# Kernel tuning notes

Hardware: AMD Instinct MI355X
Metric: run time of the kernel (lower is better)

The kernel has to match this reference:

```python
import jax, jax.numpy as jnp
import numpy as np


def setup_inputs() -> dict:
    key = jax.random.key(0)
    k1, k2, k3, k4 = jax.random.split(key, 4)
    B, S, D_IN, D_OUT = 4, 4096, 768, 128
    x = jax.random.normal(k1, (B, S, D_IN), dtype=jnp.float32)
    # torch Linear(d_in, d_out) weight is [d_out, d_in]; we store transposed [d_in, d_out]
    scale = 1.0 / np.sqrt(D_IN)
    Wq = jax.random.normal(k2, (D_IN, D_OUT), dtype=jnp.float32) * scale
    Wk = jax.random.normal(k3, (D_IN, D_OUT), dtype=jnp.float32) * scale
    Wv = jax.random.normal(k4, (D_IN, D_OUT), dtype=jnp.float32) * scale
    return {"x": x, "Wq": Wq, "Wk": Wk, "Wv": Wv}


def reference(x, Wq, Wk, Wv):
    # x: [B, S, d_in]; Wq/Wk/Wv: [d_in, d_out]
    B, S, _ = x.shape
    q = jnp.einsum('bsd,de->bse', x, Wq)
    k = jnp.einsum('bsd,de->bse', x, Wk)
    v = jnp.einsum('bsd,de->bse', x, Wv)
    d_out = k.shape[-1]
    scores = jnp.einsum('bqe,bke->bqk', q, k)  # [B, S, S]
    causal = jnp.tril(jnp.ones((S, S), dtype=bool))  # True where attention allowed
    scores = jnp.where(causal[None], scores, -jnp.inf)
    attn = jax.nn.softmax(scores / jnp.sqrt(jnp.float32(d_out)), axis=-1)
    # dropout prob is 0.0 -> identity
    return jnp.einsum('bqk,bke->bqe', attn, v)
```

## Files before the change

kernel.cpp:

```cpp
#include <hip/hip_runtime.h>
#include <stdint.h>

typedef unsigned short u16;
typedef uint32_t u32;
typedef __bf16 bf16;
typedef bf16 bf16x8 __attribute__((ext_vector_type(8)));
typedef float f32x4 __attribute__((ext_vector_type(4)));
typedef uint32_t u32x4 __attribute__((ext_vector_type(4)));

#define S_LEN 4096
#define D_IN 768
#define D_OUT 128
#define NB 4
#define M_TOTAL (NB * S_LEN)

static __device__ __forceinline__ u16 f2bf(float f) {
    union { float f; uint32_t u; } c; c.f = f;
    return (u16)((c.u + 0x7FFFu + ((c.u >> 16) & 1u)) >> 16);
}
static __device__ __forceinline__ float bf2f_lo(uint32_t w) { return __uint_as_float(w << 16); }
static __device__ __forceinline__ float bf2f_hi(uint32_t w) { return __uint_as_float(w & 0xFFFF0000u); }

static __device__ __forceinline__ bf16x8 ld8(const u16* p) {
    union { u32x4 v; bf16x8 b; } c;
    c.v = *reinterpret_cast<const u32x4*>(p);
    return c.b;
}

static __device__ __forceinline__ f32x4 mfma16(bf16x8 a, bf16x8 b, f32x4 c) {
    return __builtin_amdgcn_mfma_f32_16x16x32_bf16(a, b, c, 0, 0, 0);
}

static __device__ __forceinline__ void gload16(const void* g, void* l) {
    __builtin_amdgcn_global_load_lds((const __attribute__((address_space(1))) uint32_t*)g,
                                     (__attribute__((address_space(3))) uint32_t*)l, 16, 0, 0);
}

static __device__ __forceinline__ float bpermf(int addr, float v) {
    return __int_as_float(__builtin_amdgcn_ds_bpermute(addr, __float_as_int(v)));
}
static __device__ __forceinline__ u32 bpermu(int addr, u32 v) {
    return (u32)__builtin_amdgcn_ds_bpermute(addr, (int)v);
}
static __device__ __forceinline__ u32 pk2(float a, float b) {
    return __builtin_amdgcn_perm(__float_as_uint(b), __float_as_uint(a), 0x07060302u);
}

__global__ __launch_bounds__(256) void wt_kernel(const float* __restrict__ Wq, const float* __restrict__ Wk,
                                                 const float* __restrict__ Wv, u16* __restrict__ Wt) {
    __shared__ u16 tl[128][40];
    const int w = blockIdx.x / 24;
    const int kc = (blockIdx.x % 24) * 32;
    const float* W = (w == 0) ? Wq : (w == 1) ? Wk : Wv;
#pragma unroll
    for (int p = 0; p < 4; ++p) {
        int kr = p * 8 + (threadIdx.x >> 5);
        int nc = (threadIdx.x & 31) * 4;
        float4 v = *reinterpret_cast<const float4*>(W + (size_t)(kc + kr) * D_OUT + nc);
        tl[nc + 0][kr] = f2bf(v.x); tl[nc + 1][kr] = f2bf(v.y);
        tl[nc + 2][kr] = f2bf(v.z); tl[nc + 3][kr] = f2bf(v.w);
    }
    __syncthreads();
    const int n = threadIdx.x >> 1, kh = (threadIdx.x & 1) * 16;
    u32x4* dst = reinterpret_cast<u32x4*>(Wt + (size_t)w * D_OUT * D_IN + (size_t)n * D_IN + kc + kh);
    const u32x4* src = reinterpret_cast<const u32x4*>(&tl[n][kh]);
    dst[0] = src[0];
    dst[1] = src[1];
}

__global__ __launch_bounds__(256) void qkv_kernel(const float* __restrict__ x, const u16* __restrict__ Wt,
                                                  u16* __restrict__ Qb, u16* __restrict__ Kb,
                                                  u16* __restrict__ Vt) {
    __shared__ __align__(16) u16 wslab[2][192 * 32];
    __shared__ __align__(16) float xslab[2][64 * 32];
    const int wave = threadIdx.x >> 6, lane = threadIdx.x & 63;
    const int r = lane & 15, g = lane >> 4;
    const int m0 = blockIdx.x * 64;
    const int h = blockIdx.y;

    f32x4 acc[3][4];
#pragma unroll
    for (int y = 0; y < 3; ++y)
#pragma unroll
        for (int f = 0; f < 4; ++f) acc[y][f] = f32x4{0.f, 0.f, 0.f, 0.f};

    auto stageW = [&](int bb, int kk) {
#pragma unroll
        for (int i = 0; i < 3; ++i) {
            int c = i * 4 + wave;
            int rr = c * 16 + (lane >> 2);
            int gr = (rr >> 6) * 128 + h * 64 + (rr & 63);
            const u16* src = Wt + (size_t)gr * D_IN + kk * 32 + (((lane & 3) ^ (rr & 3)) * 8);
            gload16(src, &wslab[bb][c * 512]);
        }
    };
    auto stageX = [&](int bb, int kk) {
#pragma unroll
        for (int i = 0; i < 2; ++i) {
            int c = i * 4 + wave;
            int row = c * 8 + (lane >> 3);
            const float* src = x + (size_t)(m0 + row) * D_IN + kk * 32 + (((lane & 7) ^ (row & 7)) * 4);
            gload16(src, &xslab[bb][c * 256]);
        }
    };

    stageW(0, 0);
    stageX(0, 0);
    int buf = 0;
    const int arow = wave * 16 + r;
    for (int kk = 0; kk < 24; ++kk) {
        int kn = (kk + 1 < 24) ? kk + 1 : 0;
        stageX(buf ^ 1, kn);
        stageW(buf ^ 1, kn);
        asm volatile("s_waitcnt vmcnt(5)" ::: "memory");
        __builtin_amdgcn_sched_barrier(0);
        __builtin_amdgcn_s_barrier();
        f32x4 xa0 = *reinterpret_cast<const f32x4*>(&xslab[buf][arow * 32 + (((2 * g) ^ (arow & 7)) * 4)]);
        f32x4 xa1 = *reinterpret_cast<const f32x4*>(&xslab[buf][arow * 32 + (((2 * g + 1) ^ (arow & 7)) * 4)]);
        union { u16 u[8]; bf16x8 bv; } af;
#pragma unroll
        for (int t = 0; t < 4; ++t) { af.u[t] = f2bf(xa0[t]); af.u[4 + t] = f2bf(xa1[t]); }
#pragma unroll
        for (int y = 0; y < 3; ++y)
#pragma unroll
            for (int f = 0; f < 4; ++f) {
                int rr = y * 64 + f * 16 + r;
                bf16x8 wf = ld8(&wslab[buf][rr * 32 + ((g ^ (r & 3)) * 8)]);
                acc[y][f] = mfma16(af.bv, wf, acc[y][f]);
            }
        __builtin_amdgcn_s_barrier();
        buf ^= 1;
    }
    asm volatile("s_waitcnt vmcnt(0)" ::: "memory");

    const float QSC = 0.1275174366f;
#pragma unroll
    for (int f = 0; f < 4; ++f)
#pragma unroll
        for (int i = 0; i < 4; ++i) {
            int mrow = m0 + wave * 16 + 4 * g + i;
            int col = h * 64 + f * 16 + r;
            Qb[(size_t)mrow * D_OUT + col] = f2bf(acc[0][f][i] * QSC);
            Kb[(size_t)mrow * D_OUT + col] = f2bf(acc[1][f][i]);
            Vt[((size_t)((mrow >> 12) * D_OUT + col)) * S_LEN + (mrow & 4095)] = f2bf(acc[2][f][i]);
        }
}

__global__ __launch_bounds__(512, 2) void attn_kernel(const u16* __restrict__ Qb, const u16* __restrict__ Kb,
                                                      const u16* __restrict__ Vt, u16* __restrict__ Po,
                                                      float* __restrict__ Pml, float* __restrict__ out,
                                                      int nsplit) {
    __shared__ __align__(16) u16 kbuf[2][64 * 128];
    __shared__ __align__(16) u16 vbuf[2][128 * 64];

    const int wave = threadIdx.x >> 6, lane = threadIdx.x & 63;
    const int r = lane & 15, g = lane >> 4;
    const int n = (int)blockIdx.x;
    const int b = (n & 7) >> 1;
    const int rem = ((n >> 3) << 1) | (n & 1);
    const int s = rem >> 4;
    const int xh = rem & 15;
    const int t = (2 * s < nsplit) ? (15 - xh) : xh;
    const int nj = 4 * t + 4;
    if (s >= nj) return;
    const int qw0 = t * 256 + wave * 32;

    const u16* Kp = Kb + (size_t)b * S_LEN * D_OUT;
    const u16* Vp = Vt + (size_t)b * D_OUT * S_LEN;

    bf16x8 qf[2][4];
#pragma unroll
    for (int rb = 0; rb < 2; ++rb)
#pragma unroll
        for (int kk = 0; kk < 4; ++kk)
            qf[rb][kk] = ld8(Qb + ((size_t)(b * S_LEN + qw0 + rb * 16 + r)) * D_OUT + kk * 32 + 8 * g);

    f32x4 o[2][8];
    float l_[2];
#pragma unroll
    for (int rb = 0; rb < 2; ++rb) {
#pragma unroll
        for (int f = 0; f < 8; ++f) o[rb][f] = f32x4{0.f, 0.f, 0.f, 0.f};
        l_[rb] = 0.f;
    }

    const int la4 = (r + 32 * (g & 1)) * 4;
    const int lb4 = la4 + 64;
    const int lx16 = (lane ^ 16) * 4, lx32 = (lane ^ 32) * 4;
    const bool hi = (g >= 2);

    auto stageK = [&](int bb, int k0) {
#pragma unroll
        for (int i = 0; i < 2; ++i) {
            int c = i * 8 + wave;
            int row = c * 4 + (lane >> 4);
            const u16* src = Kp + (size_t)(k0 + row) * D_OUT + (((lane & 15) ^ (row & 7)) * 8);
            gload16(src, &kbuf[bb][c * 512]);
        }
    };
    auto stageV = [&](int bb, int k0) {
#pragma unroll
        for (int i = 0; i < 2; ++i) {
            int c = i * 8 + wave;
            int row = c * 8 + (lane >> 3);
            const u16* src = Vp + (size_t)row * S_LEN + k0 + (((lane & 7) ^ (row & 7)) * 8);
            gload16(src, &vbuf[bb][c * 512]);
        }
    };

    stageK(0, s * 64);
    stageV(0, s * 64);
    int buf = 0;
    for (int j = s; j < nj; j += nsplit) {
        const int k0 = j * 64;
        const int j2 = j + nsplit;
        const int kn = (j2 < nj) ? j2 * 64 : s * 64;
        stageK(buf ^ 1, kn);
        stageV(buf ^ 1, kn);
        asm volatile("s_waitcnt vmcnt(4)" ::: "memory");
        __builtin_amdgcn_sched_barrier(0);
        __builtin_amdgcn_s_barrier();

        f32x4 sv[2][4];
#pragma unroll
        for (int rb = 0; rb < 2; ++rb)
#pragma unroll
            for (int f = 0; f < 4; ++f) sv[rb][f] = f32x4{0.f, 0.f, 0.f, 0.f};
        __builtin_amdgcn_s_setprio(1);
#pragma unroll
        for (int kk = 0; kk < 4; ++kk)
#pragma unroll
            for (int f = 0; f < 4; ++f) {
                bf16x8 kf = ld8(&kbuf[buf][(f * 16 + r) * 128 + (((kk * 4 + g) ^ (r & 7)) * 8)]);
                sv[0][f] = mfma16(kf, qf[0][kk], sv[0][f]);
                sv[1][f] = mfma16(kf, qf[1][kk], sv[1][f]);
            }
        __builtin_amdgcn_s_setprio(0);

        bf16x8 pb[2][2];
#pragma unroll
        for (int rb = 0; rb < 2; ++rb) {
            const int qrb = qw0 + rb * 16;
            const int q = qrb + r;
            if (k0 + 63 > qrb) {
#pragma unroll
                for (int f = 0; f < 4; ++f)
#pragma unroll
                    for (int i = 0; i < 4; ++i)
                        if (k0 + 16 * f + 4 * g + i > q) sv[rb][f][i] = -1e30f;
            }
            float r0 = 0.f;
#pragma unroll
            for (int f = 0; f < 4; ++f)
#pragma unroll
                for (int i = 0; i < 4; ++i) {
                    float p = __builtin_amdgcn_exp2f(sv[rb][f][i]);
                    sv[rb][f][i] = p;
                    r0 += p;
                }
            l_[rb] += r0;

            u32 pkl[4], pkh[4];
#pragma unroll
            for (int f = 0; f < 4; ++f) {
                pkl[f] = pk2(sv[rb][f][0], sv[rb][f][1]);
                pkh[f] = pk2(sv[rb][f][2], sv[rb][f][3]);
            }
#pragma unroll
            for (int kk2 = 0; kk2 < 2; ++kk2) {
                const int f1 = 2 * kk2, f2 = 2 * kk2 + 1;
                u32 a1 = bpermu(la4, pkl[f1]), a2 = bpermu(la4, pkl[f2]);
                u32 b1 = bpermu(la4, pkh[f1]), b2 = bpermu(la4, pkh[f2]);
                u32 c1 = bpermu(lb4, pkl[f1]), c2 = bpermu(lb4, pkl[f2]);
                u32 d1 = bpermu(lb4, pkh[f1]), d2 = bpermu(lb4, pkh[f2]);
                union { u32x4 u; bf16x8 bv; } cc;
                cc.u = u32x4{hi ? a2 : a1, hi ? b2 : b1, hi ? c2 : c1, hi ? d2 : d1};
                pb[rb][kk2] = cc.bv;
            }
        }

        __builtin_amdgcn_s_setprio(1);
#pragma unroll
        for (int kk2 = 0; kk2 < 2; ++kk2)
#pragma unroll
            for (int f = 0; f < 8; ++f) {
                bf16x8 vf = ld8(&vbuf[buf][(f * 16 + r) * 64 + (((kk2 * 4 + g) ^ (r & 7)) * 8)]);
                o[0][f] = mfma16(vf, pb[0][kk2], o[0][f]);
                o[1][f] = mfma16(vf, pb[1][kk2], o[1][f]);
            }
        __builtin_amdgcn_s_setprio(0);
        __builtin_amdgcn_s_barrier();
        buf ^= 1;
    }
    asm volatile("s_waitcnt vmcnt(0)" ::: "memory");

    l_[0] += bpermf(lx16, l_[0]);
    l_[1] += bpermf(lx16, l_[1]);
    l_[0] += bpermf(lx32, l_[0]);
    l_[1] += bpermf(lx32, l_[1]);

    if (nsplit == 1) {
#pragma unroll
        for (int rb = 0; rb < 2; ++rb) {
            float inv = 1.0f / l_[rb];
            float* orow = out + ((size_t)(b * S_LEN + qw0 + rb * 16 + r)) * D_OUT;
#pragma unroll
            for (int f = 0; f < 8; ++f) {
                float4 v;
                v.x = o[rb][f][0] * inv; v.y = o[rb][f][1] * inv;
                v.z = o[rb][f][2] * inv; v.w = o[rb][f][3] * inv;
                *reinterpret_cast<float4*>(orow + 16 * f + 4 * g) = v;
            }
        }
    } else {
        const int pt = (b * 16 + t) * nsplit + s;
        u16* po = Po + (size_t)pt * (256 * 128);
        float* pml = Pml + (size_t)pt * 512;
#pragma unroll
        for (int rb = 0; rb < 2; ++rb) {
            u16* chunk0 = po + (size_t)((wave * 2 + rb) * 8) * 256 + lane * 4;
#pragma unroll
            for (int f = 0; f < 8; ++f) {
                u32 w0 = (u32)f2bf(o[rb][f][0]) | ((u32)f2bf(o[rb][f][1]) << 16);
                u32 w1 = (u32)f2bf(o[rb][f][2]) | ((u32)f2bf(o[rb][f][3]) << 16);
                uint2 ww; ww.x = w0; ww.y = w1;
                *reinterpret_cast<uint2*>(chunk0 + f * 256) = ww;
            }
            if (g == 0) {
                const int row = wave * 32 + rb * 16 + r;
                pml[row * 2 + 0] = 0.f;
                pml[row * 2 + 1] = l_[rb];
            }
        }
    }
}

__global__ __launch_bounds__(256) void merge_kernel(const u16* __restrict__ Po, const float* __restrict__ Pml,
                                                    float* __restrict__ out, int nsplit) {
    const int gr = blockIdx.x * 16 + (threadIdx.x >> 4);
    const int c0 = (threadIdx.x & 15) * 8;
    const int b = gr >> 12, rr = gr & 4095;
    const int t = rr >> 8, row = rr & 255;
    const int ns = min(nsplit, 4 * t + 4);
    const size_t pbase = (size_t)(b * 16 + t) * nsplit;

    const int wv = row >> 5, rbm = (row >> 4) & 1, r_ = row & 15;
    const int fm = c0 >> 4, g0 = (c0 >> 2) & 3;
    const size_t coff = (size_t)((wv * 2 + rbm) * 8 + fm) * 256;

    float L = 0.f;
#pragma unroll
    for (int s = 0; s < 8; ++s)
        if (s < ns) L += Pml[(pbase + s) * 512 + row * 2 + 1];
    const float inv = 1.0f / L;

    float acc[8];
#pragma unroll
    for (int k = 0; k < 8; ++k) acc[k] = 0.f;
#pragma unroll
    for (int s = 0; s < 8; ++s) {
        if (s < ns) {
            const u16* chunk = Po + (pbase + s) * (256 * 128) + coff;
            uint2 pv0 = *reinterpret_cast<const uint2*>(chunk + (g0 * 16 + r_) * 4);
            uint2 pv1 = *reinterpret_cast<const uint2*>(chunk + ((g0 + 1) * 16 + r_) * 4);
            acc[0] += bf2f_lo(pv0.x); acc[1] += bf2f_hi(pv0.x);
            acc[2] += bf2f_lo(pv0.y); acc[3] += bf2f_hi(pv0.y);
            acc[4] += bf2f_lo(pv1.x); acc[5] += bf2f_hi(pv1.x);
            acc[6] += bf2f_lo(pv1.y); acc[7] += bf2f_hi(pv1.y);
        }
    }
    float* op = out + (size_t)gr * D_OUT + c0;
    float4 v0, v1;
    v0.x = acc[0] * inv; v0.y = acc[1] * inv; v0.z = acc[2] * inv; v0.w = acc[3] * inv;
    v1.x = acc[4] * inv; v1.y = acc[5] * inv; v1.z = acc[6] * inv; v1.w = acc[7] * inv;
    *reinterpret_cast<float4*>(op) = v0;
    *reinterpret_cast<float4*>(op + 4) = v1;
}

extern "C" void kernel_launch(void* const* d_in, const int* in_sizes, int n_in,
                              void* d_out, int out_size, void* d_ws, size_t ws_size,
                              hipStream_t stream) {
    const float* x  = (const float*)d_in[0];
    const float* Wq = (const float*)d_in[1];
    const float* Wk = (const float*)d_in[2];
    const float* Wv = (const float*)d_in[3];
    float* out = (float*)d_out;

    u16* Qb = (u16*)d_ws;
    u16* Kb = Qb + (size_t)M_TOTAL * D_OUT;
    u16* Vt = Kb + (size_t)M_TOTAL * D_OUT;
    u16* Wt = Vt + (size_t)M_TOTAL * D_OUT;

    const unsigned long long base = (3ULL * M_TOTAL * D_OUT + 3ULL * D_OUT * D_IN) * 2ULL;
    const unsigned long long per = 4325376ULL;
    int nsplit = 8;
    if (ws_size < base + 8ULL * per) nsplit = 4;
    if (ws_size < base + 4ULL * per) nsplit = 2;
    if (ws_size < base + 2ULL * per) nsplit = 1;

    u16* Po = Wt + (size_t)3 * D_OUT * D_IN;
    float* Pml = (float*)(Po + (size_t)nsplit * 2097152ULL);

    wt_kernel<<<72, 256, 0, stream>>>(Wq, Wk, Wv, Wt);
    qkv_kernel<<<dim3(256, 2), 256, 0, stream>>>(x, Wt, Qb, Kb, Vt);
    attn_kernel<<<16 * nsplit * NB, 512, 0, stream>>>(Qb, Kb, Vt, Po, Pml, out, nsplit);
    if (nsplit > 1)
        merge_kernel<<<M_TOTAL / 16, 256, 0, stream>>>(Po, Pml, out, nsplit);
}
```

Baseline: 96.51 us.

## Use 16x16x16 MFMA for PV to drop bpermute shuffles; restructure prefetch

The P·V product now uses the K=16 bf16 MFMA, which accepts the QK^T accumulator layout directly as the A operand. This removes the cross-lane ds_bpermute reshuffle of the probability fragments. V fragments are read as 8-byte LDS loads with an adjusted swizzle offset. The prefetch loop is also restructured: it waits for all loads and barriers first, then issues the next stage's loads, and drops the trailing barrier and the wraparound dummy load. The trade-offs are twice as many PV MFMA instructions, narrower LDS reads, and possibly less overlap between loads and compute.

```diff
diff --git a/kernel.cpp b/kernel.cpp
--- a/kernel.cpp
+++ b/kernel.cpp
@@ -5,6 +5,8 @@
 typedef uint32_t u32;
 typedef __bf16 bf16;
 typedef bf16 bf16x8 __attribute__((ext_vector_type(8)));
+typedef bf16 bf16x4 __attribute__((ext_vector_type(4)));
+typedef short s16x4 __attribute__((ext_vector_type(4)));
 typedef float f32x4 __attribute__((ext_vector_type(4)));
 typedef uint32_t u32x4 __attribute__((ext_vector_type(4)));
 
@@ -31,6 +33,21 @@
     return __builtin_amdgcn_mfma_f32_16x16x32_bf16(a, b, c, 0, 0, 0);
 }
 
+static __device__ __forceinline__ f32x4 mfma16k16(uint2 a, uint2 b, f32x4 c) {
+#if defined(__HIP_DEVICE_COMPILE__)
+#if __has_builtin(__builtin_amdgcn_mfma_f32_16x16x16_bf16)
+    union { uint2 u; bf16x4 v; } ca, cb; ca.u = a; cb.u = b;
+    return __builtin_amdgcn_mfma_f32_16x16x16_bf16(ca.v, cb.v, c, 0, 0, 0);
+#else
+    union { uint2 u; s16x4 v; } ca, cb; ca.u = a; cb.u = b;
+    return __builtin_amdgcn_mfma_f32_16x16x16bf16_1k(ca.v, cb.v, c, 0, 0, 0);
+#endif
+#else
+    (void)a; (void)b;
+    return c;
+#endif
+}
+
 static __device__ __forceinline__ void gload16(const void* g, void* l) {
     __builtin_amdgcn_global_load_lds((const __attribute__((address_space(1))) uint32_t*)g,
                                      (__attribute__((address_space(3))) uint32_t*)l, 16, 0, 0);
@@ -38,9 +55,6 @@
 
 static __device__ __forceinline__ float bpermf(int addr, float v) {
     return __int_as_float(__builtin_amdgcn_ds_bpermute(addr, __float_as_int(v)));
-}
-static __device__ __forceinline__ u32 bpermu(int addr, u32 v) {
-    return (u32)__builtin_amdgcn_ds_bpermute(addr, (int)v);
 }
 static __device__ __forceinline__ u32 pk2(float a, float b) {
     return __builtin_amdgcn_perm(__float_as_uint(b), __float_as_uint(a), 0x07060302u);
@@ -184,10 +198,7 @@
         l_[rb] = 0.f;
     }
 
-    const int la4 = (r + 32 * (g & 1)) * 4;
-    const int lb4 = la4 + 64;
     const int lx16 = (lane ^ 16) * 4, lx32 = (lane ^ 32) * 4;
-    const bool hi = (g >= 2);
 
     auto stageK = [&](int bb, int k0) {
 #pragma unroll
@@ -213,13 +224,14 @@
     int buf = 0;
     for (int j = s; j < nj; j += nsplit) {
         const int k0 = j * 64;
-        const int j2 = j + nsplit;
-        const int kn = (j2 < nj) ? j2 * 64 : s * 64;
-        stageK(buf ^ 1, kn);
-        stageV(buf ^ 1, kn);
-        asm volatile("s_waitcnt vmcnt(4)" ::: "memory");
+        asm volatile("s_waitcnt vmcnt(0)" ::: "memory");
         __builtin_amdgcn_sched_barrier(0);
         __builtin_amdgcn_s_barrier();
+        const int j2 = j + nsplit;
+        if (j2 < nj) {
+            stageK(buf ^ 1, j2 * 64);
+            stageV(buf ^ 1, j2 * 64);
+        }
 
         f32x4 sv[2][4];
 #pragma unroll
@@ -237,7 +249,7 @@
             }
         __builtin_amdgcn_s_setprio(0);
 
-        bf16x8 pb[2][2];
+        uint2 pb[2][4];
 #pragma unroll
         for (int rb = 0; rb < 2; ++rb) {
             const int qrb = qw0 + rb * 16;
@@ -259,37 +271,25 @@
                     r0 += p;
                 }
             l_[rb] += r0;
-
-            u32 pkl[4], pkh[4];
-#pragma unroll
-            for (int f = 0; f < 4; ++f) {
-                pkl[f] = pk2(sv[rb][f][0], sv[rb][f][1]);
-                pkh[f] = pk2(sv[rb][f][2], sv[rb][f][3]);
-            }
-#pragma unroll
-            for (int kk2 = 0; kk2 < 2; ++kk2) {
-                const int f1 = 2 * kk2, f2 = 2 * kk2 + 1;
-                u32 a1 = bpermu(la4, pkl[f1]), a2 = bpermu(la4, pkl[f2]);
-                u32 b1 = bpermu(la4, pkh[f1]), b2 = bpermu(la4, pkh[f2]);
-                u32 c1 = bpermu(lb4, pkl[f1]), c2 = bpermu(lb4, pkl[f2]);
-                u32 d1 = bpermu(lb4, pkh[f1]), d2 = bpermu(lb4, pkh[f2]);
-                union { u32x4 u; bf16x8 bv; } cc;
-                cc.u = u32x4{hi ? a2 : a1, hi ? b2 : b1, hi ? c2 : c1, hi ? d2 : d1};
-                pb[rb][kk2] = cc.bv;
+#pragma unroll
+            for (int kb = 0; kb < 4; ++kb) {
+                pb[rb][kb].x = pk2(sv[rb][kb][0], sv[rb][kb][1]);
+                pb[rb][kb].y = pk2(sv[rb][kb][2], sv[rb][kb][3]);
             }
         }
 
         __builtin_amdgcn_s_setprio(1);
 #pragma unroll
-        for (int kk2 = 0; kk2 < 2; ++kk2)
+        for (int kb = 0; kb < 4; ++kb) {
+            const int vs = ((2 * kb + (g >> 1)) ^ (r & 7)) * 8 + 4 * (g & 1);
 #pragma unroll
             for (int f = 0; f < 8; ++f) {
-                bf16x8 vf = ld8(&vbuf[buf][(f * 16 + r) * 64 + (((kk2 * 4 + g) ^ (r & 7)) * 8)]);
-                o[0][f] = mfma16(vf, pb[0][kk2], o[0][f]);
-                o[1][f] = mfma16(vf, pb[1][kk2], o[1][f]);
-            }
+                uint2 vf = *reinterpret_cast<const uint2*>(&vbuf[buf][(f * 16 + r) * 64 + vs]);
+                o[0][f] = mfma16k16(vf, pb[0][kb], o[0][f]);
+                o[1][f] = mfma16k16(vf, pb[1][kb], o[1][f]);
+            }
+        }
         __builtin_amdgcn_s_setprio(0);
-        __builtin_amdgcn_s_barrier();
         buf ^= 1;
     }
     asm volatile("s_waitcnt vmcnt(0)" ::: "memory");
```

Measured after the change: 96.19 us. About the same (-0.3%).
